# Optimization experiments

Hardware: AMD Instinct MI355X
Metric: run time of the kernel (lower is better)

Reference implementation:

```python
import jax, jax.numpy as jnp
import numpy as np

TASKS = 32768          # init kwarg `tasks`
N_HEADS = TASKS + 1    # tasks + 1 distilled/shared head
IN_DIM, HID, OUT = 3, 100, 5


def setup_inputs() -> dict:
    key = jax.random.key(0)
    kx, k1, kb1, k2, kb2 = jax.random.split(key, 5)
    # per-task stacked parameters (equivalent to ModuleList of Linears)
    x = jax.random.normal(kx, (N_HEADS, IN_DIM), dtype=jnp.float32)
    # init scale ~ PyTorch default: U(-1/sqrt(fan_in), 1/sqrt(fan_in)); gaussian approx fine
    W1 = jax.random.normal(k1, (N_HEADS, HID, IN_DIM), dtype=jnp.float32) * (1.0 / np.sqrt(IN_DIM))
    b1 = jax.random.normal(kb1, (N_HEADS, HID), dtype=jnp.float32) * (1.0 / np.sqrt(IN_DIM))
    W2 = jax.random.normal(k2, (N_HEADS, OUT, HID), dtype=jnp.float32) * (1.0 / np.sqrt(HID))
    b2 = jax.random.normal(kb2, (N_HEADS, OUT), dtype=jnp.float32) * (1.0 / np.sqrt(HID))
    return {"x": x, "W1": W1, "b1": b1, "W2": W2, "b2": b2}


def reference(x, W1, b1, W2, b2):
    # x: (T+1, 3) -- one state vector per task head (matches x.view(tasks+1, -1))
    T1 = W1.shape[0]
    x = x.reshape(T1, -1)                                   # (T+1, 3)
    h = jax.nn.relu(jnp.einsum('thi,ti->th', W1, x) + b1)   # (T+1, 100)
    logits = jnp.einsum('toh,th->to', W2, h) + b2           # (T+1, 5)
    return jax.nn.softmax(logits, axis=-1)                  # (T+1, 5)
```

## Files before the change

### kernel.cpp

```cpp
#include <hip/hip_runtime.h>
#include <math.h>


#define N_HEADS 32769
#define HID     100
#define OUT     5

#define HEADS_PER_BLOCK 4
#define FLOATS_PER_HEAD 900
#define LDS_B1 300
#define LDS_W2 400

#define GLOBAL_AS __attribute__((address_space(1)))
#define LDS_AS    __attribute__((address_space(3)))

static __device__ __forceinline__ void async_copy16(const void* g, void* l) {
    __builtin_amdgcn_global_load_lds((const GLOBAL_AS void*)g, (LDS_AS void*)l,
                                     16, 0, 0);
}

__global__ __launch_bounds__(256) void distral_kernel(
    const float* __restrict__ x,
    const float* __restrict__ W1,
    const float* __restrict__ b1,
    const float* __restrict__ W2,
    const float* __restrict__ b2,
    float* __restrict__ out)
{
    __shared__ float lds[HEADS_PER_BLOCK * FLOATS_PER_HEAD];

    const int wave = threadIdx.x >> 6;
    const int lane = threadIdx.x & 63;
    const int head = blockIdx.x * HEADS_PER_BLOCK + wave;
    const bool valid = (head < N_HEADS);

    float* region = lds + wave * FLOATS_PER_HEAD;

    float x0 = 0.f, x1 = 0.f, x2 = 0.f;
    float b2v[OUT] = {0.f, 0.f, 0.f, 0.f, 0.f};

    if (valid) {
        const float* W1h = W1 + (size_t)head * 300;
        const float* b1h = b1 + (size_t)head * 100;
        const float* W2h = W2 + (size_t)head * 500;

        async_copy16(W1h + 4 * lane,            region);
        if (lane < 11)
            async_copy16(W1h + 256 + 4 * lane,  region + 256);
        if (lane < 25)
            async_copy16(b1h + 4 * lane,        region + LDS_B1);
        async_copy16(W2h + 4 * lane,            region + LDS_W2);
        if (lane < 61)
            async_copy16(W2h + 256 + 4 * lane,  region + LDS_W2 + 256);

        x0 = x[head * 3 + 0];
        x1 = x[head * 3 + 1];
        x2 = x[head * 3 + 2];
#pragma unroll
        for (int o = 0; o < OUT; ++o) b2v[o] = b2[head * OUT + o];
    }

    __syncthreads();

    if (valid) {
        const bool has2 = (lane < HID - 64);
        float h0, h1 = 0.0f;
        {
            const float* r = region + 3 * lane;
            h0 = fmaxf(fmaf(r[0], x0, fmaf(r[1], x1, fmaf(r[2], x2,
                       region[LDS_B1 + lane]))), 0.0f);
        }
        if (has2) {
            const float* r = region + 3 * (lane + 64);
            h1 = fmaxf(fmaf(r[0], x0, fmaf(r[1], x1, fmaf(r[2], x2,
                       region[LDS_B1 + lane + 64]))), 0.0f);
        }

        float acc[OUT];
#pragma unroll
        for (int o = 0; o < OUT; ++o) {
            float p = region[LDS_W2 + o * HID + lane] * h0;
            if (has2) p = fmaf(region[LDS_W2 + o * HID + 64 + lane], h1, p);
            acc[o] = p;
        }

#pragma unroll
        for (int off = 32; off > 0; off >>= 1) {
#pragma unroll
            for (int o = 0; o < OUT; ++o)
                acc[o] += __shfl_xor(acc[o], off, 64);
        }

        float m = -INFINITY;
#pragma unroll
        for (int o = 0; o < OUT; ++o) {
            acc[o] += b2v[o];
            m = fmaxf(m, acc[o]);
        }
        float s = 0.0f;
#pragma unroll
        for (int o = 0; o < OUT; ++o) {
            acc[o] = __expf(acc[o] - m);
            s += acc[o];
        }
        const float inv = 1.0f / s;

        if (lane < OUT) {
            float v = (lane == 0) ? acc[0]
                    : (lane == 1) ? acc[1]
                    : (lane == 2) ? acc[2]
                    : (lane == 3) ? acc[3]
                    :               acc[4];
            out[(size_t)head * OUT + lane] = v * inv;
        }
    }
}

extern "C" void kernel_launch(void* const* d_in, const int* in_sizes, int n_in,
                              void* d_out, int out_size, void* d_ws, size_t ws_size,
                              hipStream_t stream) {
    const float* x  = (const float*)d_in[0];
    const float* W1 = (const float*)d_in[1];
    const float* b1 = (const float*)d_in[2];
    const float* W2 = (const float*)d_in[3];
    const float* b2 = (const float*)d_in[4];
    float* out = (float*)d_out;

    const int blocks = (N_HEADS + HEADS_PER_BLOCK - 1) / HEADS_PER_BLOCK;
    distral_kernel<<<blocks, 256, 0, stream>>>(x, W1, b1, W2, b2, out);
}
```

Measured before the change: 142.3 us.

## Load W2 directly to registers, replace block barrier with waitcnt, use DPP reductions

W2 rows are now read straight into registers rather than staged through LDS, which shrinks each wave's LDS region and so the block's LDS footprint. The block-wide __syncthreads is replaced by a per-wave s_waitcnt, since each wave only reads its own LDS region; waves past the end return early. The shuffle-xor butterfly reduction is replaced by a DPP row-shift/broadcast reduction followed by readlane. The risk is correctness of the hand-coded waitcnt encoding and DPP masks, and per-wave ordering of the LDS DMA writes.

```diff
diff --git a/kernel.cpp b/kernel.cpp
--- a/kernel.cpp
+++ b/kernel.cpp
@@ -7,9 +7,8 @@
 #define OUT     5
 
 #define HEADS_PER_BLOCK 4
-#define FLOATS_PER_HEAD 900
+#define FLOATS_PER_HEAD 400
 #define LDS_B1 300
-#define LDS_W2 400
 
 #define GLOBAL_AS __attribute__((address_space(1)))
 #define LDS_AS    __attribute__((address_space(3)))
@@ -17,6 +16,27 @@
 static __device__ __forceinline__ void async_copy16(const void* g, void* l) {
     __builtin_amdgcn_global_load_lds((const GLOBAL_AS void*)g, (LDS_AS void*)l,
                                      16, 0, 0);
+}
+
+template <int CTRL, int ROW_MASK>
+static __device__ __forceinline__ float dpp_add_step(float acc) {
+    union { float f; int i; } in, out;
+    in.f = acc;
+    out.i = __builtin_amdgcn_update_dpp(0, in.i, CTRL, ROW_MASK, 0xF, false);
+    return acc + out.f;
+}
+
+static __device__ __forceinline__ float wave_reduce_add(float acc) {
+    acc = dpp_add_step<0x111, 0xF>(acc);
+    acc = dpp_add_step<0x112, 0xF>(acc);
+    acc = dpp_add_step<0x114, 0xF>(acc);
+    acc = dpp_add_step<0x118, 0xF>(acc);
+    acc = dpp_add_step<0x142, 0xA>(acc);
+    acc = dpp_add_step<0x143, 0xC>(acc);
+    union { float f; int i; } v, r;
+    v.f = acc;
+    r.i = __builtin_amdgcn_readlane(v.i, 63);
+    return r.f;
 }
 
 __global__ __launch_bounds__(256) void distral_kernel(
@@ -32,87 +52,75 @@
     const int wave = threadIdx.x >> 6;
     const int lane = threadIdx.x & 63;
     const int head = blockIdx.x * HEADS_PER_BLOCK + wave;
-    const bool valid = (head < N_HEADS);
+    if (head >= N_HEADS) return;
 
     float* region = lds + wave * FLOATS_PER_HEAD;
 
-    float x0 = 0.f, x1 = 0.f, x2 = 0.f;
-    float b2v[OUT] = {0.f, 0.f, 0.f, 0.f, 0.f};
+    const float* W1h = W1 + (size_t)head * 300;
+    const float* b1h = b1 + (size_t)head * 100;
+    async_copy16(W1h + 4 * lane,           region);
+    if (lane < 11)
+        async_copy16(W1h + 256 + 4 * lane, region + 256);
+    if (lane < 25)
+        async_copy16(b1h + 4 * lane,       region + LDS_B1);
 
-    if (valid) {
-        const float* W1h = W1 + (size_t)head * 300;
-        const float* b1h = b1 + (size_t)head * 100;
-        const float* W2h = W2 + (size_t)head * 500;
+    const float* W2h = W2 + (size_t)head * 500;
+    const bool has2 = (lane < HID - 64);
 
-        async_copy16(W1h + 4 * lane,            region);
-        if (lane < 11)
-            async_copy16(W1h + 256 + 4 * lane,  region + 256);
-        if (lane < 25)
-            async_copy16(b1h + 4 * lane,        region + LDS_B1);
-        async_copy16(W2h + 4 * lane,            region + LDS_W2);
-        if (lane < 61)
-            async_copy16(W2h + 256 + 4 * lane,  region + LDS_W2 + 256);
-
-        x0 = x[head * 3 + 0];
-        x1 = x[head * 3 + 1];
-        x2 = x[head * 3 + 2];
+    float w2a[OUT], w2b[OUT] = {0.f, 0.f, 0.f, 0.f, 0.f};
 #pragma unroll
-        for (int o = 0; o < OUT; ++o) b2v[o] = b2[head * OUT + o];
+    for (int o = 0; o < OUT; ++o)
+        w2a[o] = W2h[o * HID + lane];
+    if (has2) {
+#pragma unroll
+        for (int o = 0; o < OUT; ++o)
+            w2b[o] = W2h[o * HID + 64 + lane];
     }
 
-    __syncthreads();
+    const float x0 = x[head * 3 + 0];
+    const float x1 = x[head * 3 + 1];
+    const float x2 = x[head * 3 + 2];
+    float b2v[OUT];
+#pragma unroll
+    for (int o = 0; o < OUT; ++o) b2v[o] = b2[head * OUT + o];
 
-    if (valid) {
-        const bool has2 = (lane < HID - 64);
-        float h0, h1 = 0.0f;
-        {
-            const float* r = region + 3 * lane;
-            h0 = fmaxf(fmaf(r[0], x0, fmaf(r[1], x1, fmaf(r[2], x2,
-                       region[LDS_B1 + lane]))), 0.0f);
-        }
-        if (has2) {
-            const float* r = region + 3 * (lane + 64);
-            h1 = fmaxf(fmaf(r[0], x0, fmaf(r[1], x1, fmaf(r[2], x2,
-                       region[LDS_B1 + lane + 64]))), 0.0f);
-        }
+    __builtin_amdgcn_s_waitcnt(0x0F70);
+    asm volatile("" ::: "memory");
 
-        float acc[OUT];
+    float h0, h1 = 0.0f;
+    {
+        const float* r = region + 3 * lane;
+        h0 = fmaxf(fmaf(r[0], x0, fmaf(r[1], x1, fmaf(r[2], x2,
+                   region[LDS_B1 + lane]))), 0.0f);
+    }
+    if (has2) {
+        const float* r = region + 3 * (lane + 64);
+        h1 = fmaxf(fmaf(r[0], x0, fmaf(r[1], x1, fmaf(r[2], x2,
+                   region[LDS_B1 + lane + 64]))), 0.0f);
+    }
+
+    float logit[OUT];
 #pragma unroll
-        for (int o = 0; o < OUT; ++o) {
-            float p = region[LDS_W2 + o * HID + lane] * h0;
-            if (has2) p = fmaf(region[LDS_W2 + o * HID + 64 + lane], h1, p);
-            acc[o] = p;
-        }
+    for (int o = 0; o < OUT; ++o) {
+        float p = fmaf(w2b[o], h1, w2a[o] * h0);
+        logit[o] = wave_reduce_add(p) + b2v[o];
+    }
 
+    float m = -INFINITY;
 #pragma unroll
-        for (int off = 32; off > 0; off >>= 1) {
+    for (int o = 0; o < OUT; ++o) m = fmaxf(m, logit[o]);
+    float e[OUT], s = 0.0f;
 #pragma unroll
-            for (int o = 0; o < OUT; ++o)
-                acc[o] += __shfl_xor(acc[o], off, 64);
-        }
+    for (int o = 0; o < OUT; ++o) { e[o] = __expf(logit[o] - m); s += e[o]; }
+    const float inv = 1.0f / s;
 
-        float m = -INFINITY;
-#pragma unroll
-        for (int o = 0; o < OUT; ++o) {
-            acc[o] += b2v[o];
-            m = fmaxf(m, acc[o]);
-        }
-        float s = 0.0f;
-#pragma unroll
-        for (int o = 0; o < OUT; ++o) {
-            acc[o] = __expf(acc[o] - m);
-            s += acc[o];
-        }
-        const float inv = 1.0f / s;
-
-        if (lane < OUT) {
-            float v = (lane == 0) ? acc[0]
-                    : (lane == 1) ? acc[1]
-                    : (lane == 2) ? acc[2]
-                    : (lane == 3) ? acc[3]
-                    :               acc[4];
-            out[(size_t)head * OUT + lane] = v * inv;
-        }
+    if (lane < OUT) {
+        float v = (lane == 0) ? e[0]
+                : (lane == 1) ? e[1]
+                : (lane == 2) ? e[2]
+                : (lane == 3) ? e[3]
+                :               e[4];
+        out[(size_t)head * OUT + lane] = v * inv;
     }
 }
 
```

After: 142.8 us. No clear change (+0.3%).
